# Optimization experiments

Measured on AMD Instinct MI355X. Metric: run time of the kernel, lower is better.

## Reference

```python
import jax, jax.numpy as jnp
import numpy as np

V, D, H, HS, BLK, L = 50257, 768, 12, 64, 1024, 6
B, S = 4, 1024
EPS = 1e-5


def layer_norm(x, g, b):
    mu = jnp.mean(x, axis=-1, keepdims=True)
    var = jnp.mean(jnp.square(x - mu), axis=-1, keepdims=True)
    return (x - mu) * jax.lax.rsqrt(var + EPS) * g + b


def setup_inputs() -> dict:
    key = jax.random.key(0)
    ks = jax.random.split(key, 24)
    s = 0.02
    inp = {
        "idx": jax.random.randint(ks[0], (B, S), 0, V),
        "tok_emb": jax.random.normal(ks[1], (V, D), jnp.float32) * s,
        "pos_emb": jax.random.normal(ks[2], (BLK, D), jnp.float32) * s,
        "Wq": jax.random.normal(ks[3], (L, H, D, HS), jnp.float32) * s,
        "bq": jnp.zeros((L, H, HS), jnp.float32),
        "Wk": jax.random.normal(ks[4], (L, H, D, HS), jnp.float32) * s,
        "bk": jnp.zeros((L, H, HS), jnp.float32),
        "Wv": jax.random.normal(ks[5], (L, H, D, HS), jnp.float32) * s,
        "bv": jnp.zeros((L, H, HS), jnp.float32),
        "Wproj": jax.random.normal(ks[6], (L, D, D), jnp.float32) * s,
        "bproj": jnp.zeros((L, D), jnp.float32),
        "ln1_g": jnp.ones((L, D), jnp.float32),
        "ln1_b": jnp.zeros((L, D), jnp.float32),
        "ln2_g": jnp.ones((L, D), jnp.float32),
        "ln2_b": jnp.zeros((L, D), jnp.float32),
        "Wf1": jax.random.normal(ks[7], (L, D, 4 * D), jnp.float32) * s,
        "bf1": jnp.zeros((L, 4 * D), jnp.float32),
        "Wf2": jax.random.normal(ks[8], (L, 4 * D, D), jnp.float32) * s,
        "bf2": jnp.zeros((L, D), jnp.float32),
        "lnf_g": jnp.ones((D,), jnp.float32),
        "lnf_b": jnp.zeros((D,), jnp.float32),
        "Wlm": jax.random.normal(ks[9], (V, D), jnp.float32) * s,
    }
    return inp


def attention(x, Wq, bq, Wk, bk, Wv, bv, Wproj, bproj):
    # x: [B,S,D]; per-head projections stacked over H
    q = jnp.einsum("bsd,hdk->bhsk", x, Wq) + bq[:, None, :]
    k = jnp.einsum("bsd,hdk->bhsk", x, Wk) + bk[:, None, :]
    v = jnp.einsum("bsd,hdk->bhsk", x, Wv) + bv[:, None, :]
    scores = jnp.einsum("bhsk,bhtk->bhst", q, k)  # [B,H,S,S]
    s = x.shape[1]
    mask = jnp.tril(jnp.ones((s, s), bool))
    # original: masked_fill(-inf) THEN divide by sqrt(head_size) -- equivalent
    scores = jnp.where(mask, scores, -jnp.inf) / np.sqrt(HS)
    w = jax.nn.softmax(scores, axis=-1)
    out = jnp.einsum("bhst,bhtk->bhsk", w, v)
    out = out.transpose(0, 2, 1, 3).reshape(x.shape[0], s, H * HS)
    return out @ Wproj + bproj


def reference(idx, tok_emb, pos_emb, Wq, bq, Wk, bk, Wv, bv, Wproj, bproj,
              ln1_g, ln1_b, ln2_g, ln2_b, Wf1, bf1, Wf2, bf2, lnf_g, lnf_b, Wlm):
    s = idx.shape[1]
    x = tok_emb[idx] + pos_emb[:s]
    for i in range(L):
        h = layer_norm(x, ln1_g[i], ln1_b[i])
        x = x + attention(h, Wq[i], bq[i], Wk[i], bk[i], Wv[i], bv[i], Wproj[i], bproj[i])
        h = layer_norm(x, ln2_g[i], ln2_b[i])
        x = x + (jax.nn.gelu(h @ Wf1[i] + bf1[i], approximate=False) @ Wf2[i] + bf2[i])
    x = layer_norm(x, lnf_g, lnf_b)
    logits = x @ Wlm.T  # [B,S,V]
    return logits
```

## Files before the change

kernel.cpp:

```cpp
#include <hip/hip_runtime.h>
#include <hip/hip_bf16.h>
#include <math.h>

#define D_MODEL 768
#define N_HEAD  12
#define HEAD    64
#define SEQ     1024
#define NLAYER  6
#define BATCH   4
#define NROWS   (BATCH*SEQ)
#define VOCAB   50257
#define VPAD    50432
#define DFFN    3072
#define DQKV    2304

typedef __attribute__((ext_vector_type(8))) __bf16 bf16x8;
typedef __attribute__((ext_vector_type(4))) float f32x4;
typedef __attribute__((ext_vector_type(4))) unsigned short u16x4;

__device__ inline unsigned short f2bf(float x) {
    __hip_bfloat16 h = __float2bfloat16(x);
    return *reinterpret_cast<unsigned short*>(&h);
}

__global__ __launch_bounds__(256)
void embed_kernel(const int* __restrict__ idx, const float* __restrict__ tok,
                  const float* __restrict__ pos, float* __restrict__ x) {
    int row = blockIdx.x;
    int t = idx[row];
    int s = row & (SEQ - 1);
    const float* tp = tok + (size_t)t * D_MODEL;
    const float* pp = pos + (size_t)s * D_MODEL;
    float* xp = x + (size_t)row * D_MODEL;
    for (int i = threadIdx.x; i < D_MODEL; i += 256) xp[i] = tp[i] + pp[i];
}

__global__ __launch_bounds__(256)
void ln_kernel(const float* __restrict__ in, const float* __restrict__ gw,
               const float* __restrict__ bw, unsigned short* __restrict__ out) {
    int row = blockIdx.x;
    int tid = threadIdx.x;
    const float* x = in + (size_t)row * D_MODEL;
    float v0 = x[tid], v1 = x[tid + 256], v2 = x[tid + 512];
    float s  = v0 + v1 + v2;
    float sq = v0*v0 + v1*v1 + v2*v2;
    #pragma unroll
    for (int o = 1; o < 64; o <<= 1) { s += __shfl_xor(s, o); sq += __shfl_xor(sq, o); }
    __shared__ float red[8];
    int wave = tid >> 6;
    if ((tid & 63) == 0) { red[wave] = s; red[4 + wave] = sq; }
    __syncthreads();
    s  = red[0] + red[1] + red[2] + red[3];
    sq = red[4] + red[5] + red[6] + red[7];
    float mean = s * (1.0f / D_MODEL);
    float var  = sq * (1.0f / D_MODEL) - mean * mean;
    float rstd = rsqrtf(var + 1e-5f);
    unsigned short* op = out + (size_t)row * D_MODEL;
    op[tid]       = f2bf((v0 - mean) * rstd * gw[tid]       + bw[tid]);
    op[tid + 256] = f2bf((v1 - mean) * rstd * gw[tid + 256] + bw[tid + 256]);
    op[tid + 512] = f2bf((v2 - mean) * rstd * gw[tid + 512] + bw[tid + 512]);
}

template<int MODE>
__global__ __launch_bounds__(256)
void conv_transpose(const float* __restrict__ in, unsigned short* __restrict__ out,
                    int K, int N, size_t inLstride, size_t outLstride) {
    __shared__ float t[32][33];
    const int tx = threadIdx.x, ty = threadIdx.y;
    const int n0 = blockIdx.x * 32, k0 = blockIdx.y * 32;
    const float* ip = in + blockIdx.z * inLstride;
    unsigned short* op = out + blockIdx.z * outLstride;
    #pragma unroll
    for (int j = 0; j < 4; ++j) {
        int k = k0 + ty + j * 8, n = n0 + tx;
        float v = (MODE == 0) ? ip[(size_t)k * N + n]
                              : ip[(size_t)((n >> 6) * K + k) * 64 + (n & 63)];
        t[ty + j * 8][tx] = v;
    }
    __syncthreads();
    #pragma unroll
    for (int j = 0; j < 4; ++j) {
        int n = n0 + ty + j * 8, k = k0 + tx;
        op[(size_t)n * K + k] = f2bf(t[tx][ty + j * 8]);
    }
}

__global__ __launch_bounds__(256)
void conv_lm(const float* __restrict__ in, unsigned short* __restrict__ out) {
    const int nchunks = VPAD * D_MODEL / 4;
    const int vchunks = VOCAB * D_MODEL / 4;
    for (int i = blockIdx.x * 256 + threadIdx.x; i < nchunks; i += gridDim.x * 256) {
        u16x4 o;
        if (i < vchunks) {
            float4 v = reinterpret_cast<const float4*>(in)[i];
            o[0] = f2bf(v.x); o[1] = f2bf(v.y); o[2] = f2bf(v.z); o[3] = f2bf(v.w);
        } else { o[0] = 0; o[1] = 0; o[2] = 0; o[3] = 0; }
        reinterpret_cast<u16x4*>(out)[i] = o;
    }
}

__global__ __launch_bounds__(256)
void conv_bias(const float* __restrict__ bq, const float* __restrict__ bk,
               const float* __restrict__ bv, float* __restrict__ out) {
    int i = blockIdx.x * 256 + threadIdx.x;
    if (i >= NLAYER * DQKV) return;
    int l = i / DQKV, n = i % DQKV;
    float v;
    if (n < 768)        v = bq[l * 768 + n];
    else if (n < 1536)  v = bk[l * 768 + n - 768];
    else                v = bv[l * 768 + n - 1536];
    out[i] = v;
}

__global__ __launch_bounds__(512)
void gemm256_mfma(const unsigned short* __restrict__ A, const unsigned short* __restrict__ B,
                  float* __restrict__ C, int M, int N, int K) {
    __shared__ unsigned short smem[2 * 2 * 16384];
    const int nwg = gridDim.x;
    const int t0 = (blockIdx.x & 7) * (nwg >> 3) + (blockIdx.x >> 3);
    const int MT = M >> 8;
    const int NBX = nwg / MT;
    const int srsize = NBX * 8;
    const int sr = t0 / srsize;
    const int rem = t0 - sr * srsize;
    const int bx = rem >> 3;
    const int by = sr * 8 + (rem & 7);
    const int bm = by * 256, bn = bx * 256;
    const int tid = threadIdx.x;
    const int l = tid & 63, w = tid >> 6;
    const int wm = w >> 2, wn = w & 3;
    const int lr = l & 15, lc = l >> 4;
    f32x4 acc[8][4] = {};

    auto stage = [&](int k0, int buf) {
        #pragma unroll
        for (int p = 0; p < 4; ++p) {
            int d16 = p * 512 + tid;
            int row = d16 >> 3, cph = d16 & 7;
            int clog = cph ^ (row & 7);
            const unsigned short* ga = A + (size_t)(bm + row) * K + k0 + clog * 8;
            __builtin_amdgcn_global_load_lds(
                (const __attribute__((address_space(1))) unsigned int*)ga,
                (__attribute__((address_space(3))) unsigned int*)(&smem[buf * 32768 + d16 * 8]), 16, 0, 0);
        }
        #pragma unroll
        for (int p = 0; p < 4; ++p) {
            int d16 = p * 512 + tid;
            int row = d16 >> 3, cph = d16 & 7;
            int clog = cph ^ (row & 7);
            const unsigned short* gb = B + (size_t)(bn + row) * K + k0 + clog * 8;
            __builtin_amdgcn_global_load_lds(
                (const __attribute__((address_space(1))) unsigned int*)gb,
                (__attribute__((address_space(3))) unsigned int*)(&smem[buf * 32768 + 16384 + d16 * 8]), 16, 0, 0);
        }
    };

    auto compute = [&](int buf) {
        const unsigned short* Ab = &smem[buf * 32768];
        const unsigned short* Bb = &smem[buf * 32768 + 16384];
        #pragma unroll
        for (int qm = 0; qm < 2; ++qm) {
            bf16x8 af[2][4];
            #pragma unroll
            for (int ks = 0; ks < 2; ++ks)
                #pragma unroll
                for (int mi = 0; mi < 4; ++mi) {
                    int row = wm * 128 + qm * 64 + mi * 16 + lr;
                    af[ks][mi] = *reinterpret_cast<const bf16x8*>(
                        &Ab[row * 64 + (((ks * 4 + lc) ^ (row & 7)) * 8)]);
                }
            #pragma unroll
            for (int qn = 0; qn < 2; ++qn) {
                bf16x8 bfr[2][2];
                #pragma unroll
                for (int ks = 0; ks < 2; ++ks)
                    #pragma unroll
                    for (int ni = 0; ni < 2; ++ni) {
                        int col = wn * 64 + qn * 32 + ni * 16 + lr;
                        bfr[ks][ni] = *reinterpret_cast<const bf16x8*>(
                            &Bb[col * 64 + (((ks * 4 + lc) ^ (col & 7)) * 8)]);
                    }
                __builtin_amdgcn_s_setprio(1);
                #pragma unroll
                for (int ks = 0; ks < 2; ++ks)
                    #pragma unroll
                    for (int mi = 0; mi < 4; ++mi)
                        #pragma unroll
                        for (int ni = 0; ni < 2; ++ni)
                            acc[qm * 4 + mi][qn * 2 + ni] = __builtin_amdgcn_mfma_f32_16x16x32_bf16(
                                af[ks][mi], bfr[ks][ni], acc[qm * 4 + mi][qn * 2 + ni], 0, 0, 0);
                __builtin_amdgcn_s_setprio(0);
            }
        }
    };

    const int NT = K >> 6;
    stage(0, 0);
    asm volatile("s_waitcnt vmcnt(0)" ::: "memory");
    __builtin_amdgcn_s_barrier();
    for (int t = 0; t < NT; ++t) {
        const int cur = t & 1;
        if (t + 1 < NT) stage((t + 1) << 6, cur ^ 1);
        compute(cur);
        if (t + 1 < NT) {
            asm volatile("s_waitcnt vmcnt(0)" ::: "memory");
            __builtin_amdgcn_s_barrier();
        }
    }

    #pragma unroll
    for (int i = 0; i < 8; ++i) {
        #pragma unroll
        for (int r = 0; r < 4; ++r) {
            const int row = bm + wm * 128 + i * 16 + lc * 4 + r;
            #pragma unroll
            for (int j = 0; j < 4; ++j) {
                const int col = bn + wn * 64 + j * 16 + lr;
                if (col < N) C[(size_t)row * N + col] = acc[i][j][r];
            }
        }
    }
}

template<int BM, int OUTF , bool GELU, bool RES>
__global__ __launch_bounds__(256)
void gemm_sched(const unsigned short* __restrict__ A, const unsigned short* __restrict__ B,
                const float* __restrict__ bias, const float* __restrict__ res,
                void* __restrict__ Cout, int M, int N, int K) {
    constexpr int ABUF = BM * 64;
    constexpr int TBUF = (BM + 128) * 64;
    __shared__ unsigned short smem[2 * TBUF];
    const int nwg = gridDim.x;
    const int t0 = (blockIdx.x & 7) * (nwg >> 3) + (blockIdx.x >> 3);
    const int MT = M / BM;
    const int NBX = nwg / MT;
    const int srsize = NBX * 8;
    const int sr = t0 / srsize;
    const int rem = t0 - sr * srsize;
    const int bx = rem >> 3;
    const int by = sr * 8 + (rem & 7);
    const int bm = by * BM, bn = bx * 128;
    const int tid = threadIdx.x;
    const int l = tid & 63, w = tid >> 6;
    constexpr int MI = (BM == 128) ? 4 : 2;
    const int wr = (BM == 128) ? (w >> 1) * 64 : (w & 1) * 32;
    const int wc = (BM == 128) ? (w & 1) * 64 : (w >> 1) * 64;
    const int lr = l & 15, lc = l >> 4;
    f32x4 acc[MI][4] = {};

    auto stage = [&](int k0, int buf) {
        #pragma unroll
        for (int p = 0; p < BM * 8 / 256; ++p) {
            int d16 = p * 256 + tid;
            int row = d16 >> 3, cph = d16 & 7;
            int clog = cph ^ (row & 7);
            const unsigned short* ga = A + (size_t)(bm + row) * K + k0 + clog * 8;
            __builtin_amdgcn_global_load_lds(
                (const __attribute__((address_space(1))) unsigned int*)ga,
                (__attribute__((address_space(3))) unsigned int*)(&smem[buf * TBUF + d16 * 8]), 16, 0, 0);
        }
        #pragma unroll
        for (int p = 0; p < 4; ++p) {
            int d16 = p * 256 + tid;
            int row = d16 >> 3, cph = d16 & 7;
            int clog = cph ^ (row & 7);
            const unsigned short* gb = B + (size_t)(bn + row) * K + k0 + clog * 8;
            __builtin_amdgcn_global_load_lds(
                (const __attribute__((address_space(1))) unsigned int*)gb,
                (__attribute__((address_space(3))) unsigned int*)(&smem[buf * TBUF + ABUF + d16 * 8]), 16, 0, 0);
        }
    };

    auto compute = [&](int buf) {
        const unsigned short* Ab = &smem[buf * TBUF];
        const unsigned short* Bb = &smem[buf * TBUF + ABUF];
        #pragma unroll
        for (int ks = 0; ks < 2; ++ks) {
            bf16x8 af[MI], bfr[4];
            #pragma unroll
            for (int mi = 0; mi < MI; ++mi) {
                int row = wr + mi * 16 + lr;
                af[mi] = *reinterpret_cast<const bf16x8*>(
                    &Ab[row * 64 + (((ks * 4 + lc) ^ (row & 7)) * 8)]);
            }
            #pragma unroll
            for (int ni = 0; ni < 4; ++ni) {
                int col = wc + ni * 16 + lr;
                bfr[ni] = *reinterpret_cast<const bf16x8*>(
                    &Bb[col * 64 + (((ks * 4 + lc) ^ (col & 7)) * 8)]);
            }
            __builtin_amdgcn_s_setprio(1);
            #pragma unroll
            for (int mi = 0; mi < MI; ++mi)
                #pragma unroll
                for (int ni = 0; ni < 4; ++ni)
                    acc[mi][ni] = __builtin_amdgcn_mfma_f32_16x16x32_bf16(
                        af[mi], bfr[ni], acc[mi][ni], 0, 0, 0);
            __builtin_amdgcn_s_setprio(0);
        }
    };

    const int NT = K >> 6;
    stage(0, 0);
    asm volatile("s_waitcnt vmcnt(0)" ::: "memory");
    __builtin_amdgcn_s_barrier();
    for (int t = 0; t < NT; ++t) {
        const int cur = t & 1;
        if (t + 1 < NT) stage((t + 1) << 6, cur ^ 1);
        compute(cur);
        if (t + 1 < NT) {
            asm volatile("s_waitcnt vmcnt(0)" ::: "memory");
            __builtin_amdgcn_s_barrier();
        }
    }

    #pragma unroll
    for (int mi = 0; mi < MI; ++mi) {
        #pragma unroll
        for (int r = 0; r < 4; ++r) {
            const int row = bm + wr + mi * 16 + lc * 4 + r;
            #pragma unroll
            for (int ni = 0; ni < 4; ++ni) {
                const int col = bn + wc + ni * 16 + lr;
                float v = acc[mi][ni][r];
                if (bias) v += bias[col];
                if (GELU) v = 0.5f * v * (1.0f + erff(v * 0.70710678118654752f));
                if (RES)  v += res[(size_t)row * N + col];
                if (OUTF == 0) ((float*)Cout)[(size_t)row * N + col] = v;
                else ((unsigned short*)Cout)[(size_t)row * N + col] = f2bf(v);
            }
        }
    }
}

__global__ __launch_bounds__(512)
void attn_mfma(const unsigned short* __restrict__ qkv, unsigned short* __restrict__ ao) {
    const int qt = gridDim.x - 1 - blockIdx.x;
    const int h = blockIdx.y, b = blockIdx.z;
    const int tid = threadIdx.x;
    const int w = tid >> 6, l = tid & 63;
    const int c = l & 15, g = l >> 4;

    __shared__ unsigned short Ks[32 * 64];
    __shared__ unsigned short Vt[64 * 40];
    __shared__ unsigned int   Ps[8][16 * 20];

    const unsigned short* base = qkv + (size_t)(b * SEQ) * DQKV + h * HEAD;
    const int q0 = qt * 128 + w * 16;

    bf16x8 qf[2];
    {
        const unsigned short* qp = base + (size_t)(q0 + c) * DQKV + g * 8;
        qf[0] = *reinterpret_cast<const bf16x8*>(qp);
        qf[1] = *reinterpret_cast<const bf16x8*>(qp + 32);
    }

    f32x4 o_acc[4] = {};
    float m_run[4]  = {-INFINITY, -INFINITY, -INFINITY, -INFINITY};
    float l_run[4]  = {0.f, 0.f, 0.f, 0.f};

    const int srow = tid >> 4, sch8 = tid & 15;
    const int scj = sch8 >> 1, sh = sch8 & 1;
    const int vd = tid & 63, vw = tid >> 6;

    const int nkt = 4 * qt + 4;
    for (int kt = 0; kt < nkt; ++kt) {
        {
            const unsigned short* kp = base + (size_t)(kt * 32 + srow) * DQKV + 768 + sch8 * 4;
            u16x4 kv = *reinterpret_cast<const u16x4*>(kp);
            *reinterpret_cast<u16x4*>(&Ks[srow * 64 + ((scj ^ (srow & 7)) * 8) + sh * 4]) = kv;
        }
        {
            unsigned short vv[4];
            #pragma unroll
            for (int j = 0; j < 4; ++j)
                vv[j] = base[(size_t)(kt * 32 + vw * 4 + j) * DQKV + 1536 + vd];
            uint2 pk;
            pk.x = vv[0] | ((unsigned)vv[1] << 16);
            pk.y = vv[2] | ((unsigned)vv[3] << 16);
            *reinterpret_cast<uint2*>(&Vt[vd * 40 + vw * 4]) = pk;
        }
        __syncthreads();

        f32x4 s_acc[2] = {};
        #pragma unroll
        for (int t = 0; t < 2; ++t) {
            const int kr = t * 16 + c;
            #pragma unroll
            for (int ks = 0; ks < 2; ++ks) {
                bf16x8 kf = *reinterpret_cast<const bf16x8*>(
                    &Ks[kr * 64 + (((ks * 4 + g) ^ (kr & 7)) * 8)]);
                s_acc[t] = __builtin_amdgcn_mfma_f32_16x16x32_bf16(qf[ks], kf, s_acc[t], 0, 0, 0);
            }
        }
        float sc[2][4];
        #pragma unroll
        for (int t = 0; t < 2; ++t) {
            const int kglob = kt * 32 + t * 16 + c;
            #pragma unroll
            for (int r = 0; r < 4; ++r) {
                float v = s_acc[t][r] * 0.125f;
                sc[t][r] = (kglob > q0 + g * 4 + r) ? -1e30f : v;
            }
        }
        float pout[2][4];
        #pragma unroll
        for (int r = 0; r < 4; ++r) {
            float tmax = fmaxf(sc[0][r], sc[1][r]);
            #pragma unroll
            for (int ms = 1; ms < 16; ms <<= 1) tmax = fmaxf(tmax, __shfl_xor(tmax, ms));
            float mnew = fmaxf(m_run[r], tmax);
            float alpha = __expf(m_run[r] - mnew);
            float p0 = __expf(sc[0][r] - mnew);
            float p1 = __expf(sc[1][r] - mnew);
            float psum = p0 + p1;
            #pragma unroll
            for (int ms = 1; ms < 16; ms <<= 1) psum += __shfl_xor(psum, ms);
            l_run[r] = l_run[r] * alpha + psum;
            m_run[r] = mnew;
            #pragma unroll
            for (int dt = 0; dt < 4; ++dt) o_acc[dt][r] *= alpha;
            pout[0][r] = p0; pout[1][r] = p1;
        }
        #pragma unroll
        for (int t = 0; t < 2; ++t) {
            #pragma unroll
            for (int r = 0; r < 4; ++r) {
                int my = f2bf(pout[t][r]);
                int part = __shfl_xor(my, 1);
                unsigned int word = (c & 1) ? ((unsigned)(part & 0xffff) | ((unsigned)my << 16))
                                            : ((unsigned)(my & 0xffff) | ((unsigned)part << 16));
                Ps[w][(g * 4 + r) * 20 + t * 8 + (c >> 1)] = word;
            }
        }
        uint4 praw = *reinterpret_cast<const uint4*>(&Ps[w][c * 20 + g * 4]);
        bf16x8 pf = *reinterpret_cast<const bf16x8*>(&praw);
        #pragma unroll
        for (int dt = 0; dt < 4; ++dt) {
            bf16x8 vf = *reinterpret_cast<const bf16x8*>(&Vt[(dt * 16 + c) * 40 + g * 8]);
            o_acc[dt] = __builtin_amdgcn_mfma_f32_16x16x32_bf16(pf, vf, o_acc[dt], 0, 0, 0);
        }
        __syncthreads();
    }

    float inv[4];
    #pragma unroll
    for (int r = 0; r < 4; ++r) inv[r] = 1.0f / l_run[r];
    #pragma unroll
    for (int r = 0; r < 4; ++r) {
        unsigned short* op = ao + (size_t)(b * SEQ + q0 + g * 4 + r) * D_MODEL + h * HEAD + c;
        #pragma unroll
        for (int dt = 0; dt < 4; ++dt)
            op[dt * 16] = f2bf(o_acc[dt][r] * inv[r]);
    }
}

extern "C" void kernel_launch(void* const* d_in, const int* in_sizes, int n_in,
                              void* d_out, int out_size, void* d_ws, size_t ws_size,
                              hipStream_t stream) {
    const int*   idx     = (const int*)  d_in[0];
    const float* tok_emb = (const float*)d_in[1];
    const float* pos_emb = (const float*)d_in[2];
    const float* Wq      = (const float*)d_in[3];
    const float* bq      = (const float*)d_in[4];
    const float* Wk      = (const float*)d_in[5];
    const float* bk      = (const float*)d_in[6];
    const float* Wv      = (const float*)d_in[7];
    const float* bv      = (const float*)d_in[8];
    const float* Wproj   = (const float*)d_in[9];
    const float* bproj   = (const float*)d_in[10];
    const float* ln1g    = (const float*)d_in[11];
    const float* ln1b    = (const float*)d_in[12];
    const float* ln2g    = (const float*)d_in[13];
    const float* ln2b    = (const float*)d_in[14];
    const float* Wf1     = (const float*)d_in[15];
    const float* bf1     = (const float*)d_in[16];
    const float* Wf2     = (const float*)d_in[17];
    const float* bf2     = (const float*)d_in[18];
    const float* lnfg    = (const float*)d_in[19];
    const float* lnfb    = (const float*)d_in[20];
    const float* Wlm     = (const float*)d_in[21];
    float* outp = (float*)d_out;

    char* basep = (char*)d_ws;
    size_t off = 0;
    auto alloc = [&](size_t bytes) -> void* {
        void* p = basep + off;
        off = (off + bytes + 255) & ~(size_t)255;
        return p;
    };
    float*          x      = (float*)         alloc((size_t)NROWS * D_MODEL * 4);
    unsigned short* qkv    = (unsigned short*)alloc((size_t)NROWS * DQKV * 2);
    unsigned short* hb     = (unsigned short*)alloc((size_t)NROWS * D_MODEL * 2);
    unsigned short* ao     = (unsigned short*)alloc((size_t)NROWS * D_MODEL * 2);
    unsigned short* mid    = (unsigned short*)alloc((size_t)NROWS * DFFN * 2);
    unsigned short* Wqkvb  = (unsigned short*)alloc((size_t)NLAYER * DQKV * D_MODEL * 2);
    unsigned short* Wprojb = (unsigned short*)alloc((size_t)NLAYER * D_MODEL * D_MODEL * 2);
    unsigned short* Wf1b   = (unsigned short*)alloc((size_t)NLAYER * DFFN * D_MODEL * 2);
    unsigned short* Wf2b   = (unsigned short*)alloc((size_t)NLAYER * D_MODEL * DFFN * 2);
    unsigned short* Wlmb   = (unsigned short*)alloc((size_t)VPAD * D_MODEL * 2);
    float*          bqkv   = (float*)         alloc((size_t)NLAYER * DQKV * 4);

    dim3 blk(256);
    dim3 tblk(32, 8);

    conv_lm<<<2048, blk, 0, stream>>>(Wlm, Wlmb);
    conv_transpose<1><<<dim3(24, 24, 6), tblk, 0, stream>>>(Wq, Wqkvb,             768, 768,  (size_t)768*768,  (size_t)DQKV*768);
    conv_transpose<1><<<dim3(24, 24, 6), tblk, 0, stream>>>(Wk, Wqkvb + 768*768,   768, 768,  (size_t)768*768,  (size_t)DQKV*768);
    conv_transpose<1><<<dim3(24, 24, 6), tblk, 0, stream>>>(Wv, Wqkvb + 2*768*768, 768, 768,  (size_t)768*768,  (size_t)DQKV*768);
    conv_transpose<0><<<dim3(24, 24, 6), tblk, 0, stream>>>(Wproj, Wprojb,         768, 768,  (size_t)768*768,  (size_t)768*768);
    conv_transpose<0><<<dim3(96, 24, 6), tblk, 0, stream>>>(Wf1, Wf1b,             768, 3072, (size_t)768*3072, (size_t)3072*768);
    conv_transpose<0><<<dim3(24, 96, 6), tblk, 0, stream>>>(Wf2, Wf2b,             3072, 768, (size_t)3072*768, (size_t)768*3072);
    conv_bias<<<(NLAYER * DQKV + 255) / 256, blk, 0, stream>>>(bq, bk, bv, bqkv);

    embed_kernel<<<NROWS, blk, 0, stream>>>(idx, tok_emb, pos_emb, x);

    dim3 gqkv(32 * 18);
    dim3 g768s(64 * 6);
    dim3 g3072(32 * 24);
    dim3 ga(SEQ / 128, N_HEAD, BATCH);

    for (int li = 0; li < NLAYER; ++li) {
        ln_kernel<<<NROWS, blk, 0, stream>>>(x, ln1g + li * D_MODEL, ln1b + li * D_MODEL, hb);

        gemm_sched<128, 1, false, false><<<gqkv, blk, 0, stream>>>(
            hb, Wqkvb + (size_t)li * DQKV * D_MODEL, bqkv + li * DQKV, nullptr,
            qkv, NROWS, DQKV, D_MODEL);

        attn_mfma<<<ga, dim3(512), 0, stream>>>(qkv, ao);

        gemm_sched<64, 0, false, true><<<g768s, blk, 0, stream>>>(
            ao, Wprojb + (size_t)li * D_MODEL * D_MODEL, bproj + li * D_MODEL, x,
            x, NROWS, D_MODEL, D_MODEL);

        ln_kernel<<<NROWS, blk, 0, stream>>>(x, ln2g + li * D_MODEL, ln2b + li * D_MODEL, hb);

        gemm_sched<128, 1, true, false><<<g3072, blk, 0, stream>>>(
            hb, Wf1b + (size_t)li * DFFN * D_MODEL, bf1 + li * DFFN, nullptr,
            mid, NROWS, DFFN, D_MODEL);

        gemm_sched<64, 0, false, true><<<g768s, blk, 0, stream>>>(
            mid, Wf2b + (size_t)li * D_MODEL * DFFN, bf2 + li * D_MODEL, x,
            x, NROWS, D_MODEL, DFFN);
    }

    ln_kernel<<<NROWS, blk, 0, stream>>>(x, lnfg, lnfb, hb);

    dim3 gl((VPAD / 256) * (NROWS / 256));
    gemm256_mfma<<<gl, dim3(512), 0, stream>>>(hb, Wlmb, outp, NROWS, VOCAB, D_MODEL);
}
```

Before: 2.267 ms.

## Vectorize weight transpose, halve LM-head GEMM K-tile, vectorize GEMM epilogue

The weight-conversion transpose now uses 64x64 tiles with float4 loads and 16-byte bf16 stores, so it issues fewer and wider global accesses. The 256x256 LM-head GEMM stages a 32-wide K slice per iteration instead of 64, which halves its LDS footprint and may raise occupancy, at the cost of twice as many barriers. The generic GEMM swaps its MFMA operands so each lane holds four consecutive columns, which lets the bias, residual and output epilogue use vector loads and stores instead of scalar ones.

```diff
diff --git a/kernel.cpp b/kernel.cpp
--- a/kernel.cpp
+++ b/kernel.cpp
@@ -17,6 +17,7 @@
 typedef __attribute__((ext_vector_type(8))) __bf16 bf16x8;
 typedef __attribute__((ext_vector_type(4))) float f32x4;
 typedef __attribute__((ext_vector_type(4))) unsigned short u16x4;
+typedef __attribute__((ext_vector_type(8))) unsigned short u16x8;
 
 __device__ inline unsigned short f2bf(float x) {
     __hip_bfloat16 h = __float2bfloat16(x);
@@ -65,23 +66,32 @@
 __global__ __launch_bounds__(256)
 void conv_transpose(const float* __restrict__ in, unsigned short* __restrict__ out,
                     int K, int N, size_t inLstride, size_t outLstride) {
-    __shared__ float t[32][33];
-    const int tx = threadIdx.x, ty = threadIdx.y;
-    const int n0 = blockIdx.x * 32, k0 = blockIdx.y * 32;
+    __shared__ float t[64][65];
+    const int tid = threadIdx.x;
+    const int n0 = blockIdx.x * 64, k0 = blockIdx.y * 64;
     const float* ip = in + blockIdx.z * inLstride;
     unsigned short* op = out + blockIdx.z * outLstride;
-    #pragma unroll
-    for (int j = 0; j < 4; ++j) {
-        int k = k0 + ty + j * 8, n = n0 + tx;
-        float v = (MODE == 0) ? ip[(size_t)k * N + n]
-                              : ip[(size_t)((n >> 6) * K + k) * 64 + (n & 63)];
-        t[ty + j * 8][tx] = v;
+    {
+        const int kk = tid >> 4, nq = tid & 15;
+        #pragma unroll
+        for (int p = 0; p < 4; ++p) {
+            int k = kk + p * 16;
+            float4 v;
+            if (MODE == 0) v = *reinterpret_cast<const float4*>(&ip[(size_t)(k0 + k) * N + n0 + nq * 4]);
+            else           v = *reinterpret_cast<const float4*>(&ip[((size_t)(n0 >> 6) * K + (k0 + k)) * 64 + nq * 4]);
+            t[k][nq * 4 + 0] = v.x; t[k][nq * 4 + 1] = v.y;
+            t[k][nq * 4 + 2] = v.z; t[k][nq * 4 + 3] = v.w;
+        }
     }
     __syncthreads();
-    #pragma unroll
-    for (int j = 0; j < 4; ++j) {
-        int n = n0 + ty + j * 8, k = k0 + tx;
-        op[(size_t)n * K + k] = f2bf(t[tx][ty + j * 8]);
+    {
+        const int n = tid >> 2, kq = tid & 3;
+        unsigned short buf[16];
+        #pragma unroll
+        for (int j = 0; j < 16; ++j) buf[j] = f2bf(t[kq * 16 + j][n]);
+        unsigned short* dst = &op[(size_t)(n0 + n) * K + k0 + kq * 16];
+        *reinterpret_cast<u16x8*>(dst)     = *reinterpret_cast<u16x8*>(&buf[0]);
+        *reinterpret_cast<u16x8*>(dst + 8) = *reinterpret_cast<u16x8*>(&buf[8]);
     }
 }
 
@@ -115,7 +125,7 @@
 __global__ __launch_bounds__(512)
 void gemm256_mfma(const unsigned short* __restrict__ A, const unsigned short* __restrict__ B,
                   float* __restrict__ C, int M, int N, int K) {
-    __shared__ unsigned short smem[2 * 2 * 16384];
+    __shared__ unsigned short smem[2 * 16384];
     const int nwg = gridDim.x;
     const int t0 = (blockIdx.x & 7) * (nwg >> 3) + (blockIdx.x >> 3);
     const int MT = M >> 8;
@@ -134,73 +144,65 @@
 
     auto stage = [&](int k0, int buf) {
         #pragma unroll
-        for (int p = 0; p < 4; ++p) {
+        for (int p = 0; p < 2; ++p) {
             int d16 = p * 512 + tid;
-            int row = d16 >> 3, cph = d16 & 7;
-            int clog = cph ^ (row & 7);
+            int row = d16 >> 2, cph = d16 & 3;
+            int clog = cph ^ (row & 3);
             const unsigned short* ga = A + (size_t)(bm + row) * K + k0 + clog * 8;
             __builtin_amdgcn_global_load_lds(
                 (const __attribute__((address_space(1))) unsigned int*)ga,
-                (__attribute__((address_space(3))) unsigned int*)(&smem[buf * 32768 + d16 * 8]), 16, 0, 0);
-        }
-        #pragma unroll
-        for (int p = 0; p < 4; ++p) {
+                (__attribute__((address_space(3))) unsigned int*)(&smem[buf * 16384 + d16 * 8]), 16, 0, 0);
+        }
+        #pragma unroll
+        for (int p = 0; p < 2; ++p) {
             int d16 = p * 512 + tid;
-            int row = d16 >> 3, cph = d16 & 7;
-            int clog = cph ^ (row & 7);
+            int row = d16 >> 2, cph = d16 & 3;
+            int clog = cph ^ (row & 3);
             const unsigned short* gb = B + (size_t)(bn + row) * K + k0 + clog * 8;
             __builtin_amdgcn_global_load_lds(
                 (const __attribute__((address_space(1))) unsigned int*)gb,
-                (__attribute__((address_space(3))) unsigned int*)(&smem[buf * 32768 + 16384 + d16 * 8]), 16, 0, 0);
+                (__attribute__((address_space(3))) unsigned int*)(&smem[buf * 16384 + 8192 + d16 * 8]), 16, 0, 0);
         }
     };
 
     auto compute = [&](int buf) {
-        const unsigned short* Ab = &smem[buf * 32768];
-        const unsigned short* Bb = &smem[buf * 32768 + 16384];
+        const unsigned short* Ab = &smem[buf * 16384];
+        const unsigned short* Bb = &smem[buf * 16384 + 8192];
         #pragma unroll
         for (int qm = 0; qm < 2; ++qm) {
-            bf16x8 af[2][4];
-            #pragma unroll
-            for (int ks = 0; ks < 2; ++ks)
+            bf16x8 af[4];
+            #pragma unroll
+            for (int mi = 0; mi < 4; ++mi) {
+                int row = wm * 128 + qm * 64 + mi * 16 + lr;
+                af[mi] = *reinterpret_cast<const bf16x8*>(&Ab[row * 32 + ((lc ^ (row & 3)) * 8)]);
+            }
+            #pragma unroll
+            for (int qn = 0; qn < 2; ++qn) {
+                bf16x8 bfr[2];
                 #pragma unroll
-                for (int mi = 0; mi < 4; ++mi) {
-                    int row = wm * 128 + qm * 64 + mi * 16 + lr;
-                    af[ks][mi] = *reinterpret_cast<const bf16x8*>(
-                        &Ab[row * 64 + (((ks * 4 + lc) ^ (row & 7)) * 8)]);
+                for (int ni = 0; ni < 2; ++ni) {
+                    int col = wn * 64 + qn * 32 + ni * 16 + lr;
+                    bfr[ni] = *reinterpret_cast<const bf16x8*>(&Bb[col * 32 + ((lc ^ (col & 3)) * 8)]);
                 }
-            #pragma unroll
-            for (int qn = 0; qn < 2; ++qn) {
-                bf16x8 bfr[2][2];
-                #pragma unroll
-                for (int ks = 0; ks < 2; ++ks)
-                    #pragma unroll
-                    for (int ni = 0; ni < 2; ++ni) {
-                        int col = wn * 64 + qn * 32 + ni * 16 + lr;
-                        bfr[ks][ni] = *reinterpret_cast<const bf16x8*>(
-                            &Bb[col * 64 + (((ks * 4 + lc) ^ (col & 7)) * 8)]);
-                    }
                 __builtin_amdgcn_s_setprio(1);
                 #pragma unroll
-                for (int ks = 0; ks < 2; ++ks)
+                for (int mi = 0; mi < 4; ++mi)
                     #pragma unroll
-                    for (int mi = 0; mi < 4; ++mi)
-                        #pragma unroll
-                        for (int ni = 0; ni < 2; ++ni)
-                            acc[qm * 4 + mi][qn * 2 + ni] = __builtin_amdgcn_mfma_f32_16x16x32_bf16(
-                                af[ks][mi], bfr[ks][ni], acc[qm * 4 + mi][qn * 2 + ni], 0, 0, 0);
+                    for (int ni = 0; ni < 2; ++ni)
+                        acc[qm * 4 + mi][qn * 2 + ni] = __builtin_amdgcn_mfma_f32_16x16x32_bf16(
+                            af[mi], bfr[ni], acc[qm * 4 + mi][qn * 2 + ni], 0, 0, 0);
                 __builtin_amdgcn_s_setprio(0);
             }
         }
     };
 
-    const int NT = K >> 6;
+    const int NT = K >> 5;
     stage(0, 0);
     asm volatile("s_waitcnt vmcnt(0)" ::: "memory");
     __builtin_amdgcn_s_barrier();
     for (int t = 0; t < NT; ++t) {
         const int cur = t & 1;
-        if (t + 1 < NT) stage((t + 1) << 6, cur ^ 1);
+        if (t + 1 < NT) stage((t + 1) << 5, cur ^ 1);
         compute(cur);
         if (t + 1 < NT) {
             asm volatile("s_waitcnt vmcnt(0)" ::: "memory");
@@ -295,7 +297,7 @@
                 #pragma unroll
                 for (int ni = 0; ni < 4; ++ni)
                     acc[mi][ni] = __builtin_amdgcn_mfma_f32_16x16x32_bf16(
-                        af[mi], bfr[ni], acc[mi][ni], 0, 0, 0);
+                        bfr[ni], af[mi], acc[mi][ni], 0, 0, 0);
             __builtin_amdgcn_s_setprio(0);
         }
     };
@@ -316,18 +318,24 @@
 
     #pragma unroll
     for (int mi = 0; mi < MI; ++mi) {
-        #pragma unroll
-        for (int r = 0; r < 4; ++r) {
-            const int row = bm + wr + mi * 16 + lc * 4 + r;
-            #pragma unroll
-            for (int ni = 0; ni < 4; ++ni) {
-                const int col = bn + wc + ni * 16 + lr;
-                float v = acc[mi][ni][r];
-                if (bias) v += bias[col];
-                if (GELU) v = 0.5f * v * (1.0f + erff(v * 0.70710678118654752f));
-                if (RES)  v += res[(size_t)row * N + col];
-                if (OUTF == 0) ((float*)Cout)[(size_t)row * N + col] = v;
-                else ((unsigned short*)Cout)[(size_t)row * N + col] = f2bf(v);
+        const int row = bm + wr + mi * 16 + lr;
+        #pragma unroll
+        for (int ni = 0; ni < 4; ++ni) {
+            const int colb = bn + wc + ni * 16 + lc * 4;
+            f32x4 v = acc[mi][ni];
+            if (bias) v += *reinterpret_cast<const f32x4*>(&bias[colb]);
+            if (GELU) {
+                #pragma unroll
+                for (int r = 0; r < 4; ++r)
+                    v[r] = 0.5f * v[r] * (1.0f + erff(v[r] * 0.70710678118654752f));
+            }
+            if (RES) v += *reinterpret_cast<const f32x4*>(&res[(size_t)row * N + colb]);
+            if (OUTF == 0) {
+                *reinterpret_cast<f32x4*>(&((float*)Cout)[(size_t)row * N + colb]) = v;
+            } else {
+                u16x4 o;
+                o[0] = f2bf(v[0]); o[1] = f2bf(v[1]); o[2] = f2bf(v[2]); o[3] = f2bf(v[3]);
+                *reinterpret_cast<u16x4*>(&((unsigned short*)Cout)[(size_t)row * N + colb]) = o;
             }
         }
     }
@@ -502,15 +510,14 @@
     float*          bqkv   = (float*)         alloc((size_t)NLAYER * DQKV * 4);
 
     dim3 blk(256);
-    dim3 tblk(32, 8);
 
     conv_lm<<<2048, blk, 0, stream>>>(Wlm, Wlmb);
-    conv_transpose<1><<<dim3(24, 24, 6), tblk, 0, stream>>>(Wq, Wqkvb,             768, 768,  (size_t)768*768,  (size_t)DQKV*768);
-    conv_transpose<1><<<dim3(24, 24, 6), tblk, 0, stream>>>(Wk, Wqkvb + 768*768,   768, 768,  (size_t)768*768,  (size_t)DQKV*768);
-    conv_transpose<1><<<dim3(24, 24, 6), tblk, 0, stream>>>(Wv, Wqkvb + 2*768*768, 768, 768,  (size_t)768*768,  (size_t)DQKV*768);
-    conv_transpose<0><<<dim3(24, 24, 6), tblk, 0, stream>>>(Wproj, Wprojb,         768, 768,  (size_t)768*768,  (size_t)768*768);
-    conv_transpose<0><<<dim3(96, 24, 6), tblk, 0, stream>>>(Wf1, Wf1b,             768, 3072, (size_t)768*3072, (size_t)3072*768);
-    conv_transpose<0><<<dim3(24, 96, 6), tblk, 0, stream>>>(Wf2, Wf2b,             3072, 768, (size_t)3072*768, (size_t)768*3072);
+    conv_transpose<1><<<dim3(12, 12, 6), blk, 0, stream>>>(Wq, Wqkvb,             768, 768,  (size_t)768*768,  (size_t)DQKV*768);
+    conv_transpose<1><<<dim3(12, 12, 6), blk, 0, stream>>>(Wk, Wqkvb + 768*768,   768, 768,  (size_t)768*768,  (size_t)DQKV*768);
+    conv_transpose<1><<<dim3(12, 12, 6), blk, 0, stream>>>(Wv, Wqkvb + 2*768*768, 768, 768,  (size_t)768*768,  (size_t)DQKV*768);
+    conv_transpose<0><<<dim3(12, 12, 6), blk, 0, stream>>>(Wproj, Wprojb,         768, 768,  (size_t)768*768,  (size_t)768*768);
+    conv_transpose<0><<<dim3(48, 12, 6), blk, 0, stream>>>(Wf1, Wf1b,             768, 3072, (size_t)768*3072, (size_t)3072*768);
+    conv_transpose<0><<<dim3(12, 48, 6), blk, 0, stream>>>(Wf2, Wf2b,             3072, 768, (size_t)3072*768, (size_t)768*3072);
     conv_bias<<<(NLAYER * DQKV + 255) / 256, blk, 0, stream>>>(bq, bk, bv, bqkv);
 
     embed_kernel<<<NROWS, blk, 0, stream>>>(idx, tok_emb, pos_emb, x);
```

Result: faster. 2.122 ms (-6.4%).
